# Performance work log

Measured on AMD Instinct MI355X. Metric: run time of the kernel, lower is better.

## Reference

```python
import jax, jax.numpy as jnp
import numpy as np

B, S, D, H, HD = 4, 2048, 1024, 16, 64  # batch, seq, d_model, heads, head_dim


def setup_inputs() -> dict:
    key = jax.random.key(0)
    ks = jax.random.split(key, 9)
    scale = 0.02
    x = jax.random.normal(ks[0], (B, S, D), jnp.float32)
    Wq = jax.random.normal(ks[1], (D, H, HD), jnp.float32) * scale
    Wk = jax.random.normal(ks[2], (D, H, HD), jnp.float32) * scale
    Wv = jax.random.normal(ks[3], (D, H, HD), jnp.float32) * scale
    bq = jax.random.normal(ks[4], (H, HD), jnp.float32) * scale
    bk = jax.random.normal(ks[5], (H, HD), jnp.float32) * scale
    bv = jax.random.normal(ks[6], (H, HD), jnp.float32) * scale
    Wo = jax.random.normal(ks[7], (H, HD, D), jnp.float32) * scale
    bo = jax.random.normal(ks[8], (D,), jnp.float32) * scale
    return {"x": x, "Wq": Wq, "bq": bq, "Wk": Wk, "bk": bk,
            "Wv": Wv, "bv": bv, "Wo": Wo, "bo": bo}


def reference(x, Wq, bq, Wk, bk, Wv, bv, Wo, bo):
    # QKV projections -> (B, S, H, HD)
    q = jnp.einsum("bsd,dhe->bshe", x, Wq) + bq
    k = jnp.einsum("bsd,dhe->bshe", x, Wk) + bk
    v = jnp.einsum("bsd,dhe->bshe", x, Wv) + bv
    # scaled dot-product attention (deterministic, no mask/bias)
    q = q / jnp.sqrt(jnp.asarray(HD, q.dtype))
    scores = jnp.einsum("bqhd,bkhd->bhqk", q, k)  # (B, H, S, S)
    attn = jax.nn.softmax(scores, axis=-1)
    ctx = jnp.einsum("bhqk,bkhd->bqhd", attn, v)  # (B, S, H, HD)
    # output projection -> (B, S, D)
    return jnp.einsum("bqhd,hdo->bqo", ctx, Wo) + bo
```

## Files before the change

kernel.cpp:

```cpp
#include <hip/hip_runtime.h>


typedef unsigned short u16;
typedef __attribute__((ext_vector_type(4))) float f32x4;
typedef __attribute__((ext_vector_type(8))) short s16x8;
typedef __attribute__((ext_vector_type(4))) unsigned short u16x4;
typedef __attribute__((ext_vector_type(2))) unsigned int u32x2;
typedef __attribute__((ext_vector_type(4))) unsigned int u32x4;

#define DEV __device__ __forceinline__

#if __has_builtin(__builtin_amdgcn_exp2f)
#define EXP2(x) __builtin_amdgcn_exp2f(x)
#else
#define EXP2(x) exp2f(x)
#endif

DEV u16 f2b(float f) {
  unsigned u = __float_as_uint(f);
  u += 0x7fffu + ((u >> 16) & 1u);
  return (u16)(u >> 16);
}

DEV unsigned pack2(float a, float b) {
#if __has_builtin(__builtin_amdgcn_cvt_pk_bf16_f32)
  typedef __attribute__((ext_vector_type(2))) __bf16 bf16x2;
  bf16x2 r = __builtin_amdgcn_cvt_pk_bf16_f32(a, b);
  return __builtin_bit_cast(unsigned, r);
#else
  return (unsigned)f2b(a) | ((unsigned)f2b(b) << 16);
#endif
}

DEV void async16(const void* g, void* l) {
  __builtin_amdgcn_global_load_lds(
      (const __attribute__((address_space(1))) unsigned int*)g,
      (__attribute__((address_space(3))) unsigned int*)l, 16, 0, 0);
}

__global__ void k_cast(const float* __restrict__ x, u16* __restrict__ xb) {
  int i = (blockIdx.x * 256 + threadIdx.x) * 4;
  float4 v = *(const float4*)(x + i);
  u16x4 o;
  o.x = f2b(v.x); o.y = f2b(v.y); o.z = f2b(v.z); o.w = f2b(v.w);
  *(u16x4*)(xb + i) = o;
}

__global__ void k_packw_all(const float* __restrict__ Wq, const float* __restrict__ Wk,
                            const float* __restrict__ Wv, const float* __restrict__ Wo,
                            u16* __restrict__ wt, u16* __restrict__ wot, float qscale) {
  const float* src; u16* dst; float scale = 1.0f;
  switch (blockIdx.z) {
    case 0: src = Wq; dst = wt; scale = qscale; break;
    case 1: src = Wk; dst = wt + 1024 * 1024; break;
    case 2: src = Wv; dst = wt + 2 * 1024 * 1024; break;
    default: src = Wo; dst = wot; break;
  }
  __shared__ float tile[32][33];
  int t = threadIdx.x;
  int k0 = blockIdx.x * 32, n0 = blockIdx.y * 32;
  int c = t & 31, r0 = t >> 5;
#pragma unroll
  for (int p = 0; p < 4; ++p) {
    int r = p * 8 + r0;
    tile[r][c] = src[(size_t)(k0 + r) * 1024 + n0 + c] * scale;
  }
  __syncthreads();
#pragma unroll
  for (int p = 0; p < 4; ++p) {
    int r = p * 8 + r0;
    dst[(size_t)(n0 + r) * 1024 + k0 + c] = f2b(tile[c][r]);
  }
}

__global__ void k_packbias(const float* __restrict__ bq, const float* __restrict__ bk,
                           const float* __restrict__ bv, float* __restrict__ out,
                           float qscale) {
  int t = blockIdx.x * 256 + threadIdx.x;
  float v = (t < 1024) ? bq[t] * qscale : (t < 2048 ? bk[t - 1024] : bv[t - 2048]);
  out[t] = v;
}

template <int MODE>
__global__ __launch_bounds__(256, 2) void k_gemm_bt(
    const u16* __restrict__ A, const u16* __restrict__ Bt,
    const float* __restrict__ bias, void* __restrict__ Cout, u16* __restrict__ VT,
    int K, int ldC, int nbase) {
  __shared__ u16 SH[16384];
  u16* As = SH;
  u16* Bs = SH + 8192;
  const int t = threadIdx.x;
  const int w = t >> 6, l = t & 63;
  const int lane15 = l & 15, quad = l >> 4;
  const int m0 = blockIdx.x * 128, n0 = nbase + blockIdx.y * 128;
  const int wm = (w >> 1) * 64, wn = (w & 1) * 64;

  const int srow = t >> 3, cp = t & 7;
  const u16* aSrc[4]; const u16* bSrc[4]; int ldsOff[4];
#pragma unroll
  for (int i = 0; i < 4; ++i) {
    int row = i * 32 + srow;
    int gc = cp ^ (row & 7);
    aSrc[i] = A + (size_t)(m0 + row) * K + gc * 8;
    bSrc[i] = Bt + (size_t)(n0 + row) * K + gc * 8;
    ldsOff[i] = (i * 32 + w * 8) * 64;
  }

  f32x4 acc[4][4] = {};

  for (int kk = 0; kk < K; kk += 64) {
#pragma unroll
    for (int i = 0; i < 4; ++i) async16(aSrc[i] + kk, As + ldsOff[i]);
#pragma unroll
    for (int i = 0; i < 4; ++i) async16(bSrc[i] + kk, Bs + ldsOff[i]);
    __builtin_amdgcn_s_waitcnt(0);
    __syncthreads();

#pragma unroll
    for (int ks = 0; ks < 2; ++ks) {
      s16x8 af[4], bf[4];
#pragma unroll
      for (int mi = 0; mi < 4; ++mi) {
        int r = wm + mi * 16 + lane15;
        int c = ks * 4 + quad;
        af[mi] = *(const s16x8*)(As + r * 64 + (c ^ (r & 7)) * 8);
      }
#pragma unroll
      for (int ni = 0; ni < 4; ++ni) {
        int r = wn + ni * 16 + lane15;
        int c = ks * 4 + quad;
        bf[ni] = *(const s16x8*)(Bs + r * 64 + (c ^ (r & 7)) * 8);
      }
#pragma unroll
      for (int mi = 0; mi < 4; ++mi)
#pragma unroll
        for (int ni = 0; ni < 4; ++ni)
          acc[mi][ni] = (MODE == 0)
              ? __builtin_amdgcn_mfma_f32_16x16x32_bf16(bf[ni], af[mi], acc[mi][ni], 0, 0, 0)
              : __builtin_amdgcn_mfma_f32_16x16x32_bf16(af[mi], bf[ni], acc[mi][ni], 0, 0, 0);
    }
    __syncthreads();
  }

  if (MODE == 0) {
    u16* W = SH + w * 4096;
#pragma unroll
    for (int ni = 0; ni < 4; ++ni) {
      int gnb = n0 + wn + ni * 16 + quad * 4;
      float4 bb = *(const float4*)(bias + gnb);
#pragma unroll
      for (int mi = 0; mi < 4; ++mi) {
        int mloc = mi * 16 + lane15;
        int nloc = ni * 16 + quad * 4;
        int blk = (nloc >> 3) ^ (mloc & 7);
        u32x2 o;
        o.x = pack2(acc[mi][ni][0] + bb.x, acc[mi][ni][1] + bb.y);
        o.y = pack2(acc[mi][ni][2] + bb.z, acc[mi][ni][3] + bb.w);
        *(u32x2*)(W + mloc * 64 + blk * 8 + (quad & 1) * 4) = o;
      }
    }
    const int l8 = l & 7, lr = l >> 3;
#pragma unroll
    for (int it = 0; it < 8; ++it) {
      int mloc = it * 8 + lr;
      int lb = l8 ^ (mloc & 7);
      s16x8 v = *(const s16x8*)(W + mloc * 64 + l8 * 8);
      int gm = m0 + wm + mloc;
      *(s16x8*)((u16*)Cout + (size_t)gm * ldC + n0 + wn + lb * 8) = v;
    }
  } else if (MODE == 1) {
#pragma unroll
    for (int ni = 0; ni < 4; ++ni) {
      int gn = n0 + wn + ni * 16 + lane15;
      float bb = bias[gn];
#pragma unroll
      for (int mi = 0; mi < 4; ++mi) {
        int gmBase = m0 + wm + mi * 16 + quad * 4;
#pragma unroll
        for (int r = 0; r < 4; ++r)
          ((float*)Cout)[(size_t)(gmBase + r) * ldC + gn] = acc[mi][ni][r] + bb;
      }
    }
  } else {
    u16* W = SH + w * 4096;
#pragma unroll
    for (int ni = 0; ni < 4; ++ni) {
      int gn = n0 + wn + ni * 16 + lane15;
      float bb = bias[gn];
#pragma unroll
      for (int mi = 0; mi < 4; ++mi) {
        int nloc = ni * 16 + lane15;
        int mloc = mi * 16 + quad * 4;
        int blk = (mloc >> 3) ^ (nloc & 7);
        u32x2 o;
        o.x = pack2(acc[mi][ni][0] + bb, acc[mi][ni][1] + bb);
        o.y = pack2(acc[mi][ni][2] + bb, acc[mi][ni][3] + bb);
        *(u32x2*)(W + nloc * 64 + blk * 8 + (quad & 1) * 4) = o;
      }
    }
    const int l8 = l & 7, lr = l >> 3;
#pragma unroll
    for (int it = 0; it < 8; ++it) {
      int nloc = it * 8 + lr;
      int lb = l8 ^ (nloc & 7);
      s16x8 v = *(const s16x8*)(W + nloc * 64 + l8 * 8);
      int gv = (n0 - 2048) + wn + nloc;
      int hh = gv >> 6, hd = gv & 63;
      int gm = m0 + wm + lb * 8;
      int bb2 = gm >> 11, s = gm & 2047;
      *(s16x8*)(VT + (((size_t)(bb2 * 16 + hh) * 64 + hd) * 2048 + s)) = v;
    }
  }
}

__global__ __launch_bounds__(512, 4) void k_flash(
    const u16* __restrict__ qkv, const u16* __restrict__ vt, u16* __restrict__ ctx) {
  __shared__ u16 S[2][8192];
  const int t = threadIdx.x;
  const int w = t >> 6, l = t & 63;
  const int lane15 = l & 15, quad = l >> 4;
  const int bh = blockIdx.x, qt = blockIdx.y;
  const int b = bh >> 4, h = bh & 15;

  int qrow[2];
  s16x8 qf[2][2];
#pragma unroll
  for (int T = 0; T < 2; ++T) {
    qrow[T] = b * 2048 + qt * 256 + w * 32 + T * 16 + lane15;
    const u16* qp = qkv + (size_t)qrow[T] * 2048 + h * 64 + quad * 8;
    qf[T][0] = *(const s16x8*)(qp);
    qf[T][1] = *(const s16x8*)(qp + 32);
  }

  const int srow = t >> 3, cp = t & 7;
  const int xks = (srow & 3) | (((srow >> 3) & 1) << 2);
  const u16* kSrc = qkv + (size_t)(b * 2048 + srow) * 2048 + 1024 + h * 64 + (cp ^ xks) * 8;
  const u16* vSrc = vt + (size_t)bh * (64 * 2048) + (size_t)srow * 2048 + (cp ^ (srow & 7)) * 8;
  const int kOff = w * 512;
  const int vOff = 4096 + w * 512;

  const int kr = (lane15 >> 2) * 8 + (lane15 & 3);
  f32x4 O[2][4] = {};
  f32x4 sacc[2] = {};
  const f32x4 ZERO4 = {};
  const u32x4 onesu = {0x3F803F80u, 0x3F803F80u, 0x3F803F80u, 0x3F803F80u};
  const s16x8 onesf = __builtin_bit_cast(s16x8, onesu);

  async16(kSrc, &S[0][kOff]);
  async16(vSrc, &S[0][vOff]);

  for (int jt = 0; jt < 32; ++jt) {
    __builtin_amdgcn_s_waitcnt(0);
    __syncthreads();
    const u16* Sb = S[jt & 1];
    if (jt < 31) {
      const size_t kAdv = (size_t)(jt + 1) * 64 * 2048;
      const int vAdv = (jt + 1) * 64;
      u16* D = S[(jt & 1) ^ 1];
      async16(kSrc + kAdv, D + kOff);
      async16(vSrc + vAdv, D + vOff);
    }

    f32x4 st[2][4];
#pragma unroll
    for (int tt = 0; tt < 4; ++tt) {
      int rr = kr + (tt & 1) * 4 + (tt >> 1) * 32;
      int xk = (rr & 3) | (((rr >> 3) & 1) << 2);
      s16x8 kf = *(const s16x8*)(Sb + rr * 64 + ((0 * 4 + quad) ^ xk) * 8);
#pragma unroll
      for (int T = 0; T < 2; ++T)
        st[T][tt] = __builtin_amdgcn_mfma_f32_16x16x32_bf16(kf, qf[T][0], ZERO4, 0, 0, 0);
    }
#pragma unroll
    for (int tt = 0; tt < 4; ++tt) {
      int rr = kr + (tt & 1) * 4 + (tt >> 1) * 32;
      int xk = (rr & 3) | (((rr >> 3) & 1) << 2);
      s16x8 kf = *(const s16x8*)(Sb + rr * 64 + ((1 * 4 + quad) ^ xk) * 8);
#pragma unroll
      for (int T = 0; T < 2; ++T)
        st[T][tt] = __builtin_amdgcn_mfma_f32_16x16x32_bf16(kf, qf[T][1], st[T][tt], 0, 0, 0);
    }

#pragma unroll
    for (int ks = 0; ks < 2; ++ks) {
      s16x8 pf[2];
#pragma unroll
      for (int T = 0; T < 2; ++T) {
        float p0 = EXP2(st[T][2 * ks][0]), p1 = EXP2(st[T][2 * ks][1]);
        float p2 = EXP2(st[T][2 * ks][2]), p3 = EXP2(st[T][2 * ks][3]);
        float p4 = EXP2(st[T][2 * ks + 1][0]), p5 = EXP2(st[T][2 * ks + 1][1]);
        float p6 = EXP2(st[T][2 * ks + 1][2]), p7 = EXP2(st[T][2 * ks + 1][3]);
        u32x4 pu = {pack2(p0, p1), pack2(p2, p3), pack2(p4, p5), pack2(p6, p7)};
        pf[T] = __builtin_bit_cast(s16x8, pu);
        sacc[T] = __builtin_amdgcn_mfma_f32_16x16x32_bf16(onesf, pf[T], sacc[T], 0, 0, 0);
      }
      const u16* Vh = Sb + 4096;
      int c7 = ks * 4 + quad;
#pragma unroll
      for (int co = 0; co < 4; ++co) {
        int rr = co * 16 + lane15;
        s16x8 vf = *(const s16x8*)(Vh + rr * 64 + ((c7 ^ (rr & 7))) * 8);
#pragma unroll
        for (int T = 0; T < 2; ++T)
          O[T][co] = __builtin_amdgcn_mfma_f32_16x16x32_bf16(vf, pf[T], O[T][co], 0, 0, 0);
      }
    }
  }

#pragma unroll
  for (int T = 0; T < 2; ++T) {
    float inv = 1.0f / sacc[T][0];
#pragma unroll
    for (int co = 0; co < 4; ++co) {
      u32x2 o;
      o.x = pack2(O[T][co][0] * inv, O[T][co][1] * inv);
      o.y = pack2(O[T][co][2] * inv, O[T][co][3] * inv);
      *(u32x2*)(ctx + (size_t)qrow[T] * 1024 + h * 64 + co * 16 + quad * 4) = o;
    }
  }
}

static constexpr size_t OFF_XB  = 0;
static constexpr size_t OFF_WT  = OFF_XB + (16u << 20);
static constexpr size_t OFF_WOT = OFF_WT + (6u << 20);
static constexpr size_t OFF_B3  = OFF_WOT + (2u << 20);
static constexpr size_t OFF_QKV = OFF_B3 + (1u << 20);
static constexpr size_t OFF_VT  = OFF_QKV + (32u << 20);
static constexpr size_t OFF_CTX = OFF_VT + (16u << 20);

extern "C" void kernel_launch(void* const* d_in, const int* in_sizes, int n_in,
                              void* d_out, int out_size, void* d_ws, size_t ws_size,
                              hipStream_t stream) {
  const float* x  = (const float*)d_in[0];
  const float* Wq = (const float*)d_in[1];
  const float* bq = (const float*)d_in[2];
  const float* Wk = (const float*)d_in[3];
  const float* bk = (const float*)d_in[4];
  const float* Wv = (const float*)d_in[5];
  const float* bv = (const float*)d_in[6];
  const float* Wo = (const float*)d_in[7];
  const float* bo = (const float*)d_in[8];
  char* ws = (char*)d_ws;
  u16* xb    = (u16*)(ws + OFF_XB);
  u16* wt    = (u16*)(ws + OFF_WT);
  u16* wot   = (u16*)(ws + OFF_WOT);
  float* b3  = (float*)(ws + OFF_B3);
  u16* qkv   = (u16*)(ws + OFF_QKV);
  u16* vtb   = (u16*)(ws + OFF_VT);
  u16* ctx   = (u16*)(ws + OFF_CTX);
  float* out = (float*)d_out;

  const float QSCALE = 0.125f * 1.44269504f;

  k_cast<<<8192, 256, 0, stream>>>(x, xb);
  k_packw_all<<<dim3(32, 32, 4), 256, 0, stream>>>(Wq, Wk, Wv, Wo, wt, wot, QSCALE);
  k_packbias<<<12, 256, 0, stream>>>(bq, bk, bv, b3, QSCALE);
  k_gemm_bt<0><<<dim3(64, 16), 256, 0, stream>>>(xb, wt, b3, qkv, nullptr, 1024, 2048, 0);
  k_gemm_bt<2><<<dim3(64, 8), 256, 0, stream>>>(xb, wt, b3, nullptr, vtb, 1024, 2048, 2048);
  k_flash<<<dim3(64, 8), 512, 0, stream>>>(qkv, vtb, ctx);
  k_gemm_bt<1><<<dim3(64, 8), 256, 0, stream>>>(ctx, wot, bo, out, nullptr, 1024, 1024, 0);
}
```

Measured before the change: 272.8 us.

## Double K/V tile per barrier, use scalar row sums, add MFMA priority hints

```diff
diff --git a/kernel.cpp b/kernel.cpp
--- a/kernel.cpp
+++ b/kernel.cpp
@@ -215,7 +215,7 @@
 
 __global__ __launch_bounds__(512, 4) void k_flash(
     const u16* __restrict__ qkv, const u16* __restrict__ vt, u16* __restrict__ ctx) {
-  __shared__ u16 S[2][8192];
+  __shared__ u16 S[2][16384];
   const int t = threadIdx.x;
   const int w = t >> 6, l = t & 63;
   const int lane15 = l & 15, quad = l >> 4;
@@ -236,80 +236,97 @@
   const int xks = (srow & 3) | (((srow >> 3) & 1) << 2);
   const u16* kSrc = qkv + (size_t)(b * 2048 + srow) * 2048 + 1024 + h * 64 + (cp ^ xks) * 8;
   const u16* vSrc = vt + (size_t)bh * (64 * 2048) + (size_t)srow * 2048 + (cp ^ (srow & 7)) * 8;
-  const int kOff = w * 512;
-  const int vOff = 4096 + w * 512;
+  const int kOff0 = w * 512,         kOff1 = 4096 + w * 512;
+  const int vOff0 = 8192 + w * 512,  vOff1 = 12288 + w * 512;
 
   const int kr = (lane15 >> 2) * 8 + (lane15 & 3);
   f32x4 O[2][4] = {};
-  f32x4 sacc[2] = {};
+  float lsum[2] = {0.0f, 0.0f};
   const f32x4 ZERO4 = {};
-  const u32x4 onesu = {0x3F803F80u, 0x3F803F80u, 0x3F803F80u, 0x3F803F80u};
-  const s16x8 onesf = __builtin_bit_cast(s16x8, onesu);
-
-  async16(kSrc, &S[0][kOff]);
-  async16(vSrc, &S[0][vOff]);
-
-  for (int jt = 0; jt < 32; ++jt) {
+
+  async16(kSrc, &S[0][kOff0]);
+  async16(kSrc + 64 * 2048, &S[0][kOff1]);
+  async16(vSrc, &S[0][vOff0]);
+  async16(vSrc + 64, &S[0][vOff1]);
+
+  for (int jt = 0; jt < 16; ++jt) {
     __builtin_amdgcn_s_waitcnt(0);
     __syncthreads();
     const u16* Sb = S[jt & 1];
-    if (jt < 31) {
-      const size_t kAdv = (size_t)(jt + 1) * 64 * 2048;
-      const int vAdv = (jt + 1) * 64;
+    if (jt < 15) {
+      const size_t kAdv = (size_t)(jt + 1) * 128 * 2048;
+      const int vAdv = (jt + 1) * 128;
       u16* D = S[(jt & 1) ^ 1];
-      async16(kSrc + kAdv, D + kOff);
-      async16(vSrc + vAdv, D + vOff);
-    }
-
-    f32x4 st[2][4];
-#pragma unroll
-    for (int tt = 0; tt < 4; ++tt) {
-      int rr = kr + (tt & 1) * 4 + (tt >> 1) * 32;
-      int xk = (rr & 3) | (((rr >> 3) & 1) << 2);
-      s16x8 kf = *(const s16x8*)(Sb + rr * 64 + ((0 * 4 + quad) ^ xk) * 8);
-#pragma unroll
-      for (int T = 0; T < 2; ++T)
-        st[T][tt] = __builtin_amdgcn_mfma_f32_16x16x32_bf16(kf, qf[T][0], ZERO4, 0, 0, 0);
-    }
-#pragma unroll
-    for (int tt = 0; tt < 4; ++tt) {
-      int rr = kr + (tt & 1) * 4 + (tt >> 1) * 32;
-      int xk = (rr & 3) | (((rr >> 3) & 1) << 2);
-      s16x8 kf = *(const s16x8*)(Sb + rr * 64 + ((1 * 4 + quad) ^ xk) * 8);
-#pragma unroll
-      for (int T = 0; T < 2; ++T)
-        st[T][tt] = __builtin_amdgcn_mfma_f32_16x16x32_bf16(kf, qf[T][1], st[T][tt], 0, 0, 0);
-    }
-
-#pragma unroll
-    for (int ks = 0; ks < 2; ++ks) {
-      s16x8 pf[2];
-#pragma unroll
-      for (int T = 0; T < 2; ++T) {
-        float p0 = EXP2(st[T][2 * ks][0]), p1 = EXP2(st[T][2 * ks][1]);
-        float p2 = EXP2(st[T][2 * ks][2]), p3 = EXP2(st[T][2 * ks][3]);
-        float p4 = EXP2(st[T][2 * ks + 1][0]), p5 = EXP2(st[T][2 * ks + 1][1]);
-        float p6 = EXP2(st[T][2 * ks + 1][2]), p7 = EXP2(st[T][2 * ks + 1][3]);
-        u32x4 pu = {pack2(p0, p1), pack2(p2, p3), pack2(p4, p5), pack2(p6, p7)};
-        pf[T] = __builtin_bit_cast(s16x8, pu);
-        sacc[T] = __builtin_amdgcn_mfma_f32_16x16x32_bf16(onesf, pf[T], sacc[T], 0, 0, 0);
-      }
-      const u16* Vh = Sb + 4096;
-      int c7 = ks * 4 + quad;
-#pragma unroll
-      for (int co = 0; co < 4; ++co) {
-        int rr = co * 16 + lane15;
-        s16x8 vf = *(const s16x8*)(Vh + rr * 64 + ((c7 ^ (rr & 7))) * 8);
+      async16(kSrc + kAdv, D + kOff0);
+      async16(kSrc + kAdv + 64 * 2048, D + kOff1);
+      async16(vSrc + vAdv, D + vOff0);
+      async16(vSrc + vAdv + 64, D + vOff1);
+    }
+
+#pragma unroll
+    for (int sub = 0; sub < 2; ++sub) {
+      const u16* Kb = Sb + sub * 4096;
+      const u16* Vb = Sb + 8192 + sub * 4096;
+
+      f32x4 st[2][4];
+      __builtin_amdgcn_s_setprio(1);
+#pragma unroll
+      for (int tt = 0; tt < 4; ++tt) {
+        int rr = kr + (tt & 1) * 4 + (tt >> 1) * 32;
+        int xk = (rr & 3) | (((rr >> 3) & 1) << 2);
+        s16x8 kf = *(const s16x8*)(Kb + rr * 64 + ((0 * 4 + quad) ^ xk) * 8);
 #pragma unroll
         for (int T = 0; T < 2; ++T)
-          O[T][co] = __builtin_amdgcn_mfma_f32_16x16x32_bf16(vf, pf[T], O[T][co], 0, 0, 0);
+          st[T][tt] = __builtin_amdgcn_mfma_f32_16x16x32_bf16(kf, qf[T][0], ZERO4, 0, 0, 0);
+      }
+#pragma unroll
+      for (int tt = 0; tt < 4; ++tt) {
+        int rr = kr + (tt & 1) * 4 + (tt >> 1) * 32;
+        int xk = (rr & 3) | (((rr >> 3) & 1) << 2);
+        s16x8 kf = *(const s16x8*)(Kb + rr * 64 + ((1 * 4 + quad) ^ xk) * 8);
+#pragma unroll
+        for (int T = 0; T < 2; ++T)
+          st[T][tt] = __builtin_amdgcn_mfma_f32_16x16x32_bf16(kf, qf[T][1], st[T][tt], 0, 0, 0);
+      }
+      __builtin_amdgcn_s_setprio(0);
+
+#pragma unroll
+      for (int ks = 0; ks < 2; ++ks) {
+        s16x8 pf[2];
+#pragma unroll
+        for (int T = 0; T < 2; ++T) {
+          float p0 = EXP2(st[T][2 * ks][0]), p1 = EXP2(st[T][2 * ks][1]);
+          float p2 = EXP2(st[T][2 * ks][2]), p3 = EXP2(st[T][2 * ks][3]);
+          float p4 = EXP2(st[T][2 * ks + 1][0]), p5 = EXP2(st[T][2 * ks + 1][1]);
+          float p6 = EXP2(st[T][2 * ks + 1][2]), p7 = EXP2(st[T][2 * ks + 1][3]);
+          lsum[T] += ((p0 + p1) + (p2 + p3)) + ((p4 + p5) + (p6 + p7));
+          u32x4 pu = {pack2(p0, p1), pack2(p2, p3), pack2(p4, p5), pack2(p6, p7)};
+          pf[T] = __builtin_bit_cast(s16x8, pu);
+        }
+        int c7 = ks * 4 + quad;
+        __builtin_amdgcn_s_setprio(1);
+#pragma unroll
+        for (int co = 0; co < 4; ++co) {
+          int rr = co * 16 + lane15;
+          s16x8 vf = *(const s16x8*)(Vb + rr * 64 + ((c7 ^ (rr & 7))) * 8);
+#pragma unroll
+          for (int T = 0; T < 2; ++T)
+            O[T][co] = __builtin_amdgcn_mfma_f32_16x16x32_bf16(vf, pf[T], O[T][co], 0, 0, 0);
+        }
+        __builtin_amdgcn_s_setprio(0);
       }
     }
   }
 
 #pragma unroll
   for (int T = 0; T < 2; ++T) {
-    float inv = 1.0f / sacc[T][0];
+    lsum[T] += __shfl_xor(lsum[T], 16);
+    lsum[T] += __shfl_xor(lsum[T], 32);
+  }
+
+#pragma unroll
+  for (int T = 0; T < 2; ++T) {
+    float inv = 1.0f / lsum[T];
 #pragma unroll
     for (int co = 0; co < 4; ++co) {
       u32x2 o;
```

New measurement: 555.0 us. 103% more time.
